# Kernel optimization log

Hardware: AMD Instinct MI355X
Metric: run time of the kernel (lower is better)

The kernel has to match this reference:

```python
import jax, jax.numpy as jnp
import numpy as np

N, E, H, NUM_RBF = 50000, 800000, 32, 32
D_IN = 2 * (NUM_RBF + H)  # 128: att_src(H) + att_dst(H) + rbf(2*NUM_RBF)
LN_EPS = 1e-5


def _decompose(t):
    # irreducible decomposition of [..., 3, 3] tensor
    eye = jnp.eye(3, dtype=t.dtype)
    I = jnp.mean(jnp.diagonal(t, axis1=-2, axis2=-1), axis=-1)[..., None, None] * eye
    A = 0.5 * (t - jnp.swapaxes(t, -1, -2))
    S = 0.5 * (t + jnp.swapaxes(t, -1, -2)) - I
    return I, A, S


def _tnorm(t):
    # squared Frobenius norm over last two dims -> [..., H]
    return (t ** 2).sum((-2, -1))


def _chan_lin(t, W):
    # nn.Linear over channel dim: t [N,H,3,3], W [H_out,H_in]
    return jnp.einsum('nhij,gh->ngij', t, W)


def setup_inputs() -> dict:
    key = jax.random.key(0)
    ks = jax.random.split(key, 12)

    def lin(k, o, i):
        return (jax.random.normal(k, (o, i), jnp.float32) / np.sqrt(i)).astype(jnp.float32)

    return {
        'X': jax.random.normal(ks[0], (N, H, 3, 3), jnp.float32),
        'rbf': jax.random.normal(ks[1], (E, 2 * NUM_RBF), jnp.float32),
        'dist': jax.random.uniform(ks[2], (E,), jnp.float32),
        'src': jax.random.randint(ks[3], (E,), 0, N),
        'dst': jax.random.randint(ks[4], (E,), 0, N),
        'Ws0': lin(ks[5], H, D_IN), 'b0': jnp.zeros((H,), jnp.float32),
        'Ws1': lin(ks[6], 2 * H, H), 'b1': jnp.zeros((2 * H,), jnp.float32),
        'Ws2': lin(ks[7], 3 * H, 2 * H), 'b2': jnp.zeros((3 * H,), jnp.float32),
        'Wt': (jax.random.normal(ks[8], (6, H, H), jnp.float32) / np.sqrt(H)).astype(jnp.float32),
        'ln_w': jnp.ones((3 * H,), jnp.float32), 'ln_b': jnp.zeros((3 * H,), jnp.float32),
        'lin_w': lin(ks[9], H, 3 * H), 'lin_b': jnp.zeros((H,), jnp.float32),
    }


def reference(X, rbf, dist, src, dst, Ws0, b0, Ws1, b1, Ws2, b2, Wt, ln_w, ln_b, lin_w, lin_b):
    n = X.shape[0]
    act = jax.nn.silu

    # atom_inf branch: per-node scalar attributes from tensor norms
    I, A, S = _decompose(X)
    x = jnp.concatenate([_tnorm(I), _tnorm(A), _tnorm(S)], axis=-1)  # [N, 3H]
    mu = x.mean(-1, keepdims=True)
    var = x.var(-1, keepdims=True)
    x = (x - mu) / jnp.sqrt(var + LN_EPS) * ln_w + ln_b
    att = act(x @ lin_w.T + lin_b)  # [N, H]

    # edge features: cat(att[src], att[dst], rbf) -> scalar MLP
    e = jnp.concatenate([att[src], att[dst], rbf], axis=-1)  # [E, D_IN]
    e = act(e @ Ws0.T + b0)
    e = act(e @ Ws1.T + b1)
    e = act(e @ Ws2.T + b2)  # [E, 3H]
    C = jnp.ones_like(dist)  # original code overwrites cutoff with ones
    e = (e * C[:, None]).reshape(e.shape[0], H, 3)  # [E, H, 3]

    # normalize node tensors, decompose, per-channel linear mix
    Xn = X / (_tnorm(X) + 1.0)[..., None, None]
    I, A, S = _decompose(Xn)
    I = _chan_lin(I, Wt[0])
    A = _chan_lin(A, Wt[1])
    S = _chan_lin(S, Wt[2])
    Y = I + A + S

    # tensor message passing: gather src, scale by edge factor, scatter-sum to dst
    def mp(T, f):
        return jax.ops.segment_sum(T[src] * f[:, :, None, None], dst, num_segments=n)

    msg = mp(I, e[..., 0]) + mp(A, e[..., 1]) + mp(S, e[..., 2])

    # O(3) group
    B1 = jnp.matmul(msg, Y)
    B2 = jnp.matmul(Y, msg)
    I, A, S = _decompose(B1 + B2)

    normp1 = (_tnorm(I + A + S) + 1.0)[..., None, None]
    I, A, S = I / normp1, A / normp1, S / normp1
    I = _chan_lin(I, Wt[3])
    A = _chan_lin(A, Wt[4])
    S = _chan_lin(S, Wt[5])
    dX = I + A + S
    X_out = Xn + dX + jnp.matmul(dX, dX)  # matrix_power(dX, 2)
    return X_out, e
```

## Files before the change

kernel.cpp:

```cpp
#include <hip/hip_runtime.h>
#include <math.h>

#define HC 32
#define NODE_PER_BLK 8

typedef _Float16 half8 __attribute__((ext_vector_type(8)));
typedef float float4v __attribute__((ext_vector_type(4)));

__device__ __forceinline__ float silu_f(float x) { return x / (1.0f + __expf(-x)); }

__device__ __forceinline__ unsigned int pk2(float a, float b) {
    union { _Float16 h[2]; unsigned int u; } t;
    t.h[0] = (_Float16)a; t.h[1] = (_Float16)b;
    return t.u;
}
__device__ __forceinline__ void unpk2(unsigned int u, float& a, float& b) {
    union { unsigned int u; _Float16 h[2]; } t;
    t.u = u;
    a = (float)t.h[0]; b = (float)t.h[1];
}

__device__ __forceinline__ void recon3(const float* c, float* T) {
    T[0] = c[0] + c[4];  T[1] = c[1] + c[5];  T[2] = c[2] + c[6];
    T[3] = -c[1] + c[5]; T[4] = c[0] + c[7];  T[5] = c[3] + c[8];
    T[6] = -c[2] + c[6]; T[7] = -c[3] + c[8]; T[8] = c[0] - c[4] - c[7];
}

__global__ void prep_weights(const float* __restrict__ Ws0, const float* __restrict__ Ws1,
                             const float* __restrict__ Ws2,
                             _Float16* __restrict__ wf1, _Float16* __restrict__ wf2,
                             _Float16* __restrict__ wf3) {
    int t = blockIdx.x * 256 + threadIdx.x;
    int j = t & 7;
    int lane = (t >> 3) & 63;
    int q = lane >> 4, r = lane & 15;
    if (t < 4096) {
        int fi = t >> 9, kt = fi >> 1, nt = fi & 1;
        wf1[t] = (_Float16)Ws0[(16 * nt + r) * 128 + 32 * kt + 8 * q + j];
    } else if (t < 6144) {
        int t2 = t - 4096;
        int nt = t2 >> 9;
        wf2[t2] = (_Float16)Ws1[(16 * nt + r) * 32 + 8 * q + j];
    } else if (t < 12288) {
        int t3 = t - 6144;
        int fi = t3 >> 9, kt = fi / 6, nt = fi % 6;
        wf3[t3] = (_Float16)Ws2[(16 * nt + r) * 64 + 32 * kt + 8 * q + j];
    }
}

__global__ void hist_kernel(const int* __restrict__ dst, int* __restrict__ cnt, int E) {
    int e = blockIdx.x * 256 + threadIdx.x;
    if (e < E) atomicAdd(&cnt[dst[e]], 1);
}

__global__ __launch_bounds__(1024) void scan_kernel(const int* __restrict__ cnt,
                                                    int* __restrict__ off,
                                                    int* __restrict__ cursor, int N) {
    __shared__ int s[1024];
    int carry = 0;
    for (int base = 0; base < N; base += 1024) {
        int i = base + threadIdx.x;
        int v = (i < N) ? cnt[i] : 0;
        s[threadIdx.x] = v;
        __syncthreads();
        #pragma unroll
        for (int o = 1; o < 1024; o <<= 1) {
            int t = (threadIdx.x >= o) ? s[threadIdx.x - o] : 0;
            __syncthreads();
            s[threadIdx.x] += t;
            __syncthreads();
        }
        int inc = s[threadIdx.x];
        int total = s[1023];
        if (i < N) {
            int ex = carry + inc - v;
            off[i] = ex;
            cursor[i] = ex;
        }
        __syncthreads();
        carry += total;
    }
    if (threadIdx.x == 0) off[N] = carry;
}

__global__ void scatter_kernel(const int* __restrict__ src, const int* __restrict__ dst,
                               int* __restrict__ cursor, int2* __restrict__ elist, int E) {
    int e = blockIdx.x * 256 + threadIdx.x;
    if (e >= E) return;
    int d = dst[e];
    int pos = atomicAdd(&cursor[d], 1);
    elist[pos] = make_int2(e, src[e]);
}

__global__ void node_prep(const float* __restrict__ X,
                          const float* __restrict__ lin_w, const float* __restrict__ lin_b,
                          const float* __restrict__ ln_w, const float* __restrict__ ln_b,
                          const float* __restrict__ Wt,
                          float* __restrict__ att, unsigned int* __restrict__ comp_g, int N) {
    __shared__ float sX[NODE_PER_BLK][96];
    __shared__ float sC[NODE_PER_BLK][HC * 9];
    int grp = threadIdx.x >> 5;
    int lane = threadIdx.x & 31;
    int n = blockIdx.x * NODE_PER_BLK + grp;
    bool valid = (n < N);

    float m = 0, a01 = 0, a02 = 0, a12 = 0, s00 = 0, s01 = 0, s02 = 0, s11 = 0, s12 = 0, s22 = 0;
    float tI = 0, tA = 0, tS = 0, tX = 0;
    if (valid) {
        const float* xp = X + (size_t)n * 288 + lane * 9;
        float t00 = xp[0], t01 = xp[1], t02 = xp[2];
        float t10 = xp[3], t11 = xp[4], t12 = xp[5];
        float t20 = xp[6], t21 = xp[7], t22 = xp[8];
        m = (t00 + t11 + t22) * (1.0f / 3.0f);
        a01 = 0.5f * (t01 - t10); a02 = 0.5f * (t02 - t20); a12 = 0.5f * (t12 - t21);
        s00 = t00 - m; s11 = t11 - m; s22 = t22 - m;
        s01 = 0.5f * (t01 + t10); s02 = 0.5f * (t02 + t20); s12 = 0.5f * (t12 + t21);
        tI = 3.0f * m * m;
        tA = 2.0f * (a01 * a01 + a02 * a02 + a12 * a12);
        tS = s00 * s00 + s11 * s11 + s22 * s22 + 2.0f * (s01 * s01 + s02 * s02 + s12 * s12);
        tX = tI + tA + tS;
    }
    float lsum = tI + tA + tS;
    #pragma unroll
    for (int o = 16; o; o >>= 1) lsum += __shfl_xor(lsum, o, 32);
    float mu = lsum * (1.0f / 96.0f);
    float d0 = tI - mu, d1 = tA - mu, d2 = tS - mu;
    float lsq = d0 * d0 + d1 * d1 + d2 * d2;
    #pragma unroll
    for (int o = 16; o; o >>= 1) lsq += __shfl_xor(lsq, o, 32);
    float rstd = rsqrtf(lsq * (1.0f / 96.0f) + 1e-5f);
    if (valid) {
        sX[grp][lane]      = d0 * rstd * ln_w[lane]      + ln_b[lane];
        sX[grp][32 + lane] = d1 * rstd * ln_w[32 + lane] + ln_b[32 + lane];
        sX[grp][64 + lane] = d2 * rstd * ln_w[64 + lane] + ln_b[64 + lane];
    }
    __syncthreads();
    if (valid) {
        float acc = lin_b[lane];
        const float* wr = lin_w + lane * 96;
        #pragma unroll
        for (int k = 0; k < 96; k++) acc += wr[k] * sX[grp][k];
        att[(size_t)n * 32 + lane] = silu_f(acc);
        float inv = 1.0f / (tX + 1.0f);
        float* cc = &sC[grp][lane * 9];
        cc[0] = m * inv;
        cc[1] = a01 * inv; cc[2] = a02 * inv; cc[3] = a12 * inv;
        cc[4] = s00 * inv; cc[5] = s01 * inv; cc[6] = s02 * inv;
        cc[7] = s11 * inv; cc[8] = s12 * inv;
    }
    __syncthreads();
    if (valid) {
        float o[9];
        #pragma unroll
        for (int c = 0; c < 9; c++) o[c] = 0.0f;
        const float* w0 = Wt + lane * 32;
        const float* w1 = Wt + 1024 + lane * 32;
        const float* w2 = Wt + 2048 + lane * 32;
        #pragma unroll
        for (int h = 0; h < 32; h++) {
            float wi = w0[h], wa = w1[h], ws = w2[h];
            const float* ch = &sC[grp][h * 9];
            o[0] += wi * ch[0];
            o[1] += wa * ch[1]; o[2] += wa * ch[2]; o[3] += wa * ch[3];
            o[4] += ws * ch[4]; o[5] += ws * ch[5]; o[6] += ws * ch[6];
            o[7] += ws * ch[7]; o[8] += ws * ch[8];
        }
        unsigned int* cgp = comp_g + (size_t)n * 160 + lane;
        cgp[0]   = pk2(o[0], o[1]);
        cgp[32]  = pk2(o[2], o[3]);
        cgp[64]  = pk2(o[4], o[5]);
        cgp[96]  = pk2(o[6], o[7]);
        cgp[128] = pk2(o[8], 0.0f);
    }
}

__device__ __forceinline__ half8 cvt8(const float* p) {
    half8 h;
    #pragma unroll
    for (int j = 0; j < 8; j++) h[j] = (_Float16)p[j];
    return h;
}

__global__ __launch_bounds__(256) void edge_mfma(
    const float* __restrict__ att, const float* __restrict__ rbf,
    const int* __restrict__ src, const int* __restrict__ dst,
    const _Float16* __restrict__ wf1, const _Float16* __restrict__ wf2,
    const _Float16* __restrict__ wf3,
    const float* __restrict__ b0, const float* __restrict__ b1, const float* __restrict__ b2,
    float* __restrict__ e_out, int E) {
    __shared__ _Float16 hbuf[4][16][72];
    int w = threadIdx.x >> 6;
    int lane = threadIdx.x & 63;
    int q = lane >> 4, r = lane & 15;
    int ebase = blockIdx.x * 64 + w * 16;
    int er = min(ebase + r, E - 1);
    int s = src[er], d = dst[er];

    half8 a0 = cvt8(att + (size_t)s * 32 + 8 * q);
    half8 a1 = cvt8(att + (size_t)d * 32 + 8 * q);
    half8 a2 = cvt8(rbf + (size_t)er * 64 + 8 * q);
    half8 a3 = cvt8(rbf + (size_t)er * 64 + 32 + 8 * q);

    const half8* W1 = (const half8*)wf1;
    float bn0 = b0[r], bn1 = b0[16 + r];
    float4v acc10 = {bn0, bn0, bn0, bn0};
    float4v acc11 = {bn1, bn1, bn1, bn1};
    acc10 = __builtin_amdgcn_mfma_f32_16x16x32_f16(a0, W1[0 * 64 + lane], acc10, 0, 0, 0);
    acc11 = __builtin_amdgcn_mfma_f32_16x16x32_f16(a0, W1[1 * 64 + lane], acc11, 0, 0, 0);
    acc10 = __builtin_amdgcn_mfma_f32_16x16x32_f16(a1, W1[2 * 64 + lane], acc10, 0, 0, 0);
    acc11 = __builtin_amdgcn_mfma_f32_16x16x32_f16(a1, W1[3 * 64 + lane], acc11, 0, 0, 0);
    acc10 = __builtin_amdgcn_mfma_f32_16x16x32_f16(a2, W1[4 * 64 + lane], acc10, 0, 0, 0);
    acc11 = __builtin_amdgcn_mfma_f32_16x16x32_f16(a2, W1[5 * 64 + lane], acc11, 0, 0, 0);
    acc10 = __builtin_amdgcn_mfma_f32_16x16x32_f16(a3, W1[6 * 64 + lane], acc10, 0, 0, 0);
    acc11 = __builtin_amdgcn_mfma_f32_16x16x32_f16(a3, W1[7 * 64 + lane], acc11, 0, 0, 0);
    #pragma unroll
    for (int reg = 0; reg < 4; reg++) {
        hbuf[w][4 * q + reg][r]      = (_Float16)silu_f(acc10[reg]);
        hbuf[w][4 * q + reg][16 + r] = (_Float16)silu_f(acc11[reg]);
    }

    half8 ah1 = *(const half8*)&hbuf[w][r][8 * q];
    const half8* W2 = (const half8*)wf2;
    float4v acc2[4];
    #pragma unroll
    for (int nt = 0; nt < 4; nt++) {
        float bb = b1[16 * nt + r];
        acc2[nt] = (float4v){bb, bb, bb, bb};
        acc2[nt] = __builtin_amdgcn_mfma_f32_16x16x32_f16(ah1, W2[nt * 64 + lane], acc2[nt], 0, 0, 0);
    }
    #pragma unroll
    for (int nt = 0; nt < 4; nt++) {
        #pragma unroll
        for (int reg = 0; reg < 4; reg++) {
            hbuf[w][4 * q + reg][16 * nt + r] = (_Float16)silu_f(acc2[nt][reg]);
        }
    }

    half8 ah20 = *(const half8*)&hbuf[w][r][8 * q];
    half8 ah21 = *(const half8*)&hbuf[w][r][32 + 8 * q];
    const half8* W3 = (const half8*)wf3;
    float4v acc3[6];
    #pragma unroll
    for (int nt = 0; nt < 6; nt++) {
        float bb = b2[16 * nt + r];
        acc3[nt] = (float4v){bb, bb, bb, bb};
        acc3[nt] = __builtin_amdgcn_mfma_f32_16x16x32_f16(ah20, W3[nt * 64 + lane], acc3[nt], 0, 0, 0);
        acc3[nt] = __builtin_amdgcn_mfma_f32_16x16x32_f16(ah21, W3[(6 + nt) * 64 + lane], acc3[nt], 0, 0, 0);
    }
    #pragma unroll
    for (int nt = 0; nt < 6; nt++) {
        #pragma unroll
        for (int reg = 0; reg < 4; reg++) {
            int ee = ebase + 4 * q + reg;
            if (ee < E) e_out[(size_t)ee * 96 + 16 * nt + r] = silu_f(acc3[nt][reg]);
        }
    }
}

__global__ void gather_final(const float* __restrict__ X,
                             const unsigned int* __restrict__ comp_g,
                             const float* __restrict__ e_out,
                             const int* __restrict__ off, const int2* __restrict__ elist,
                             const float* __restrict__ Wt,
                             float* __restrict__ Xout, int N) {
    __shared__ float sB[NODE_PER_BLK][HC * 9];
    int grp = threadIdx.x >> 5;
    int lane = threadIdx.x & 31;
    int n = blockIdx.x * NODE_PER_BLK + grp;
    bool valid = (n < N);

    float cm[9];
    #pragma unroll
    for (int c = 0; c < 9; c++) cm[c] = 0.0f;

    if (valid) {
        int start = off[n], end = off[n + 1];
        for (int idx = start; idx < end; idx++) {
            int2 es = elist[idx];
            const float* ep = e_out + (size_t)es.x * 96 + lane * 3;
            float e0 = ep[0], e1 = ep[1], e2 = ep[2];
            const unsigned int* cg = comp_g + (size_t)es.y * 160 + lane;
            float c0, c1, c2, c3, c4, c5, c6, c7, c8, cz;
            unpk2(cg[0], c0, c1);
            unpk2(cg[32], c2, c3);
            unpk2(cg[64], c4, c5);
            unpk2(cg[96], c6, c7);
            unpk2(cg[128], c8, cz);
            cm[0] += e0 * c0;
            cm[1] += e1 * c1; cm[2] += e1 * c2; cm[3] += e1 * c3;
            cm[4] += e2 * c4; cm[5] += e2 * c5; cm[6] += e2 * c6;
            cm[7] += e2 * c7; cm[8] += e2 * c8;
        }
    }

    if (valid) {
        float cy[9], cz;
        const unsigned int* cgn = comp_g + (size_t)n * 160 + lane;
        unpk2(cgn[0], cy[0], cy[1]);
        unpk2(cgn[32], cy[2], cy[3]);
        unpk2(cgn[64], cy[4], cy[5]);
        unpk2(cgn[96], cy[6], cy[7]);
        unpk2(cgn[128], cy[8], cz);
        float M[9], Y[9];
        recon3(cm, M);
        recon3(cy, Y);
        float B[9];
        #pragma unroll
        for (int i = 0; i < 3; i++) {
            #pragma unroll
            for (int j = 0; j < 3; j++) {
                float acc = 0.0f;
                #pragma unroll
                for (int k = 0; k < 3; k++)
                    acc += M[i * 3 + k] * Y[k * 3 + j] + Y[i * 3 + k] * M[k * 3 + j];
                B[i * 3 + j] = acc;
            }
        }
        float mB = (B[0] + B[4] + B[8]) * (1.0f / 3.0f);
        float tn = 1.0f;
        #pragma unroll
        for (int i = 0; i < 9; i++) tn += B[i] * B[i];
        float itn = 1.0f / tn;
        float* bb = &sB[grp][lane * 9];
        bb[0] = mB * itn;
        bb[1] = 0.5f * (B[1] - B[3]) * itn;
        bb[2] = 0.5f * (B[2] - B[6]) * itn;
        bb[3] = 0.5f * (B[5] - B[7]) * itn;
        bb[4] = (B[0] - mB) * itn;
        bb[5] = 0.5f * (B[1] + B[3]) * itn;
        bb[6] = 0.5f * (B[2] + B[6]) * itn;
        bb[7] = (B[4] - mB) * itn;
        bb[8] = 0.5f * (B[5] + B[7]) * itn;
    }
    __syncthreads();
    if (valid) {
        float o[9];
        #pragma unroll
        for (int c = 0; c < 9; c++) o[c] = 0.0f;
        const float* w3 = Wt + 3 * 1024 + lane * 32;
        const float* w4 = Wt + 4 * 1024 + lane * 32;
        const float* w5 = Wt + 5 * 1024 + lane * 32;
        #pragma unroll
        for (int h = 0; h < 32; h++) {
            float wi = w3[h], wa = w4[h], ws = w5[h];
            const float* ch = &sB[grp][h * 9];
            o[0] += wi * ch[0];
            o[1] += wa * ch[1]; o[2] += wa * ch[2]; o[3] += wa * ch[3];
            o[4] += ws * ch[4]; o[5] += ws * ch[5]; o[6] += ws * ch[6];
            o[7] += ws * ch[7]; o[8] += ws * ch[8];
        }
        float D[9];
        recon3(o, D);
        const float* xp = X + (size_t)n * 288 + lane * 9;
        float xv[9];
        float t = 0.0f;
        #pragma unroll
        for (int i = 0; i < 9; i++) { xv[i] = xp[i]; t += xv[i] * xv[i]; }
        float inv = 1.0f / (t + 1.0f);
        float P[9];
        #pragma unroll
        for (int i = 0; i < 3; i++) {
            #pragma unroll
            for (int j = 0; j < 3; j++) {
                float acc = 0.0f;
                #pragma unroll
                for (int k = 0; k < 3; k++) acc += D[i * 3 + k] * D[k * 3 + j];
                P[i * 3 + j] = acc;
            }
        }
        float* op = Xout + (size_t)n * 288 + lane * 9;
        #pragma unroll
        for (int i = 0; i < 9; i++) op[i] = xv[i] * inv + D[i] + P[i];
    }
}

extern "C" void kernel_launch(void* const* d_in, const int* in_sizes, int n_in,
                              void* d_out, int out_size, void* d_ws, size_t ws_size,
                              hipStream_t stream) {
    const float* X = (const float*)d_in[0];
    const float* rbf = (const float*)d_in[1];
    const int* src = (const int*)d_in[3];
    const int* dst = (const int*)d_in[4];
    const float* Ws0 = (const float*)d_in[5];
    const float* b0 = (const float*)d_in[6];
    const float* Ws1 = (const float*)d_in[7];
    const float* b1 = (const float*)d_in[8];
    const float* Ws2 = (const float*)d_in[9];
    const float* b2 = (const float*)d_in[10];
    const float* Wt = (const float*)d_in[11];
    const float* ln_w = (const float*)d_in[12];
    const float* ln_b = (const float*)d_in[13];
    const float* lin_w = (const float*)d_in[14];
    const float* lin_b = (const float*)d_in[15];

    int N = in_sizes[0] / 288;
    int E = in_sizes[1] / 64;

    float* Xout = (float*)d_out;
    float* e_out = (float*)d_out + (size_t)N * 288;

    float* att = (float*)d_ws;
    unsigned int* comp_g = (unsigned int*)(att + (size_t)N * 32);
    _Float16* wf1 = (_Float16*)(comp_g + (size_t)N * 160);
    _Float16* wf2 = wf1 + 4096;
    _Float16* wf3 = wf2 + 2048;
    int* cnt = (int*)(wf3 + 6144);
    int* off = cnt + N;
    int* cursor = off + N + 1;
    int2* elist = (int2*)(cursor + N + 1);

    hipMemsetAsync(cnt, 0, (size_t)N * sizeof(int), stream);
    prep_weights<<<48, 256, 0, stream>>>(Ws0, Ws1, Ws2, wf1, wf2, wf3);
    node_prep<<<(N + NODE_PER_BLK - 1) / NODE_PER_BLK, 256, 0, stream>>>(
        X, lin_w, lin_b, ln_w, ln_b, Wt, att, comp_g, N);
    hist_kernel<<<(E + 255) / 256, 256, 0, stream>>>(dst, cnt, E);
    scan_kernel<<<1, 1024, 0, stream>>>(cnt, off, cursor, N);
    scatter_kernel<<<(E + 255) / 256, 256, 0, stream>>>(src, dst, cursor, elist, E);
    edge_mfma<<<(E + 63) / 64, 256, 0, stream>>>(
        att, rbf, src, dst, wf1, wf2, wf3, b0, b1, b2, e_out, E);
    gather_final<<<(N + NODE_PER_BLK - 1) / NODE_PER_BLK, 256, 0, stream>>>(
        X, comp_g, e_out, off, elist, Wt, Xout, N);
}
```

Baseline: 704.2 us.

## Parallelize offset scan across blocks and split node edge gather across warps

Replaces the single-block serial prefix scan over node degrees with a three-pass multi-block scan (block sums, scan of sums, local scan plus offset). Reworks the gather kernel to assign one block per destination node, with eight warps striding over its incoming edges and reducing partial messages in shared memory. This targets the serial latency of the one-block scan and the per-node sequential edge loop. In exchange it adds two extra launches, launches one block per node, and leaves seven warps idle during the per-node epilogue.

```diff
diff --git a/kernel.cpp b/kernel.cpp
--- a/kernel.cpp
+++ b/kernel.cpp
@@ -53,34 +53,57 @@
     if (e < E) atomicAdd(&cnt[dst[e]], 1);
 }
 
-__global__ __launch_bounds__(1024) void scan_kernel(const int* __restrict__ cnt,
-                                                    int* __restrict__ off,
-                                                    int* __restrict__ cursor, int N) {
+__global__ __launch_bounds__(1024) void scan_a(const int* __restrict__ cnt,
+                                               int* __restrict__ bsum, int N) {
     __shared__ int s[1024];
-    int carry = 0;
-    for (int base = 0; base < N; base += 1024) {
-        int i = base + threadIdx.x;
-        int v = (i < N) ? cnt[i] : 0;
-        s[threadIdx.x] = v;
+    int i = blockIdx.x * 1024 + threadIdx.x;
+    s[threadIdx.x] = (i < N) ? cnt[i] : 0;
+    __syncthreads();
+    #pragma unroll
+    for (int o = 512; o; o >>= 1) {
+        if (threadIdx.x < o) s[threadIdx.x] += s[threadIdx.x + o];
         __syncthreads();
-        #pragma unroll
-        for (int o = 1; o < 1024; o <<= 1) {
-            int t = (threadIdx.x >= o) ? s[threadIdx.x - o] : 0;
-            __syncthreads();
-            s[threadIdx.x] += t;
-            __syncthreads();
-        }
-        int inc = s[threadIdx.x];
-        int total = s[1023];
-        if (i < N) {
-            int ex = carry + inc - v;
-            off[i] = ex;
-            cursor[i] = ex;
-        }
+    }
+    if (threadIdx.x == 0) bsum[blockIdx.x] = s[0];
+}
+
+__global__ __launch_bounds__(1024) void scan_b(int* __restrict__ bsum, int nb) {
+    __shared__ int s[1024];
+    int v = (threadIdx.x < nb) ? bsum[threadIdx.x] : 0;
+    s[threadIdx.x] = v;
+    __syncthreads();
+    #pragma unroll
+    for (int o = 1; o < 1024; o <<= 1) {
+        int t = (threadIdx.x >= o) ? s[threadIdx.x - o] : 0;
         __syncthreads();
-        carry += total;
-    }
-    if (threadIdx.x == 0) off[N] = carry;
+        s[threadIdx.x] += t;
+        __syncthreads();
+    }
+    if (threadIdx.x < nb) bsum[threadIdx.x] = s[threadIdx.x] - v;
+}
+
+__global__ __launch_bounds__(1024) void scan_c(const int* __restrict__ cnt,
+                                               const int* __restrict__ bsum,
+                                               int* __restrict__ off,
+                                               int* __restrict__ cursor, int N) {
+    __shared__ int s[1024];
+    int i = blockIdx.x * 1024 + threadIdx.x;
+    int v = (i < N) ? cnt[i] : 0;
+    s[threadIdx.x] = v;
+    __syncthreads();
+    #pragma unroll
+    for (int o = 1; o < 1024; o <<= 1) {
+        int t = (threadIdx.x >= o) ? s[threadIdx.x - o] : 0;
+        __syncthreads();
+        s[threadIdx.x] += t;
+        __syncthreads();
+    }
+    int ex = bsum[blockIdx.x] + s[threadIdx.x] - v;
+    if (i < N) {
+        off[i] = ex;
+        cursor[i] = ex;
+        if (i == N - 1) off[N] = ex + v;
+    }
 }
 
 __global__ void scatter_kernel(const int* __restrict__ src, const int* __restrict__ dst,
@@ -257,43 +280,53 @@
     }
 }
 
-__global__ void gather_final(const float* __restrict__ X,
-                             const unsigned int* __restrict__ comp_g,
-                             const float* __restrict__ e_out,
-                             const int* __restrict__ off, const int2* __restrict__ elist,
-                             const float* __restrict__ Wt,
-                             float* __restrict__ Xout, int N) {
-    __shared__ float sB[NODE_PER_BLK][HC * 9];
+__global__ __launch_bounds__(256) void gather_final(
+    const float* __restrict__ X, const unsigned int* __restrict__ comp_g,
+    const float* __restrict__ e_out,
+    const int* __restrict__ off, const int2* __restrict__ elist,
+    const float* __restrict__ Wt, float* __restrict__ Xout, int N) {
+    __shared__ float sM[8][288];
+    __shared__ float sB[288];
+    int n = blockIdx.x;
     int grp = threadIdx.x >> 5;
     int lane = threadIdx.x & 31;
-    int n = blockIdx.x * NODE_PER_BLK + grp;
-    bool valid = (n < N);
+    int start = off[n], end = off[n + 1];
 
     float cm[9];
     #pragma unroll
     for (int c = 0; c < 9; c++) cm[c] = 0.0f;
 
-    if (valid) {
-        int start = off[n], end = off[n + 1];
-        for (int idx = start; idx < end; idx++) {
-            int2 es = elist[idx];
-            const float* ep = e_out + (size_t)es.x * 96 + lane * 3;
-            float e0 = ep[0], e1 = ep[1], e2 = ep[2];
-            const unsigned int* cg = comp_g + (size_t)es.y * 160 + lane;
-            float c0, c1, c2, c3, c4, c5, c6, c7, c8, cz;
-            unpk2(cg[0], c0, c1);
-            unpk2(cg[32], c2, c3);
-            unpk2(cg[64], c4, c5);
-            unpk2(cg[96], c6, c7);
-            unpk2(cg[128], c8, cz);
-            cm[0] += e0 * c0;
-            cm[1] += e1 * c1; cm[2] += e1 * c2; cm[3] += e1 * c3;
-            cm[4] += e2 * c4; cm[5] += e2 * c5; cm[6] += e2 * c6;
-            cm[7] += e2 * c7; cm[8] += e2 * c8;
-        }
-    }
-
-    if (valid) {
+    for (int idx = start + grp; idx < end; idx += 8) {
+        int2 es = elist[idx];
+        const float* ep = e_out + (size_t)es.x * 96 + lane * 3;
+        float e0 = ep[0], e1 = ep[1], e2 = ep[2];
+        const unsigned int* cg = comp_g + (size_t)es.y * 160 + lane;
+        float c0, c1, c2, c3, c4, c5, c6, c7, c8, cz;
+        unpk2(cg[0], c0, c1);
+        unpk2(cg[32], c2, c3);
+        unpk2(cg[64], c4, c5);
+        unpk2(cg[96], c6, c7);
+        unpk2(cg[128], c8, cz);
+        cm[0] += e0 * c0;
+        cm[1] += e1 * c1; cm[2] += e1 * c2; cm[3] += e1 * c3;
+        cm[4] += e2 * c4; cm[5] += e2 * c5; cm[6] += e2 * c6;
+        cm[7] += e2 * c7; cm[8] += e2 * c8;
+    }
+    #pragma unroll
+    for (int c = 0; c < 9; c++) sM[grp][lane * 9 + c] = cm[c];
+    __syncthreads();
+    for (int t = threadIdx.x; t < 288; t += 256) {
+        float s = sM[0][t];
+        #pragma unroll
+        for (int g = 1; g < 8; g++) s += sM[g][t];
+        sM[0][t] = s;
+    }
+    __syncthreads();
+
+    if (grp == 0) {
+        float cmt[9];
+        #pragma unroll
+        for (int c = 0; c < 9; c++) cmt[c] = sM[0][lane * 9 + c];
         float cy[9], cz;
         const unsigned int* cgn = comp_g + (size_t)n * 160 + lane;
         unpk2(cgn[0], cy[0], cy[1]);
@@ -302,7 +335,7 @@
         unpk2(cgn[96], cy[6], cy[7]);
         unpk2(cgn[128], cy[8], cz);
         float M[9], Y[9];
-        recon3(cm, M);
+        recon3(cmt, M);
         recon3(cy, Y);
         float B[9];
         #pragma unroll
@@ -321,7 +354,7 @@
         #pragma unroll
         for (int i = 0; i < 9; i++) tn += B[i] * B[i];
         float itn = 1.0f / tn;
-        float* bb = &sB[grp][lane * 9];
+        float* bb = &sB[lane * 9];
         bb[0] = mB * itn;
         bb[1] = 0.5f * (B[1] - B[3]) * itn;
         bb[2] = 0.5f * (B[2] - B[6]) * itn;
@@ -333,7 +366,7 @@
         bb[8] = 0.5f * (B[5] + B[7]) * itn;
     }
     __syncthreads();
-    if (valid) {
+    if (grp == 0) {
         float o[9];
         #pragma unroll
         for (int c = 0; c < 9; c++) o[c] = 0.0f;
@@ -343,7 +376,7 @@
         #pragma unroll
         for (int h = 0; h < 32; h++) {
             float wi = w3[h], wa = w4[h], ws = w5[h];
-            const float* ch = &sB[grp][h * 9];
+            const float* ch = &sB[h * 9];
             o[0] += wi * ch[0];
             o[1] += wa * ch[1]; o[2] += wa * ch[2]; o[3] += wa * ch[3];
             o[4] += ws * ch[4]; o[5] += ws * ch[5]; o[6] += ws * ch[6];
@@ -353,10 +386,10 @@
         recon3(o, D);
         const float* xp = X + (size_t)n * 288 + lane * 9;
         float xv[9];
-        float t = 0.0f;
-        #pragma unroll
-        for (int i = 0; i < 9; i++) { xv[i] = xp[i]; t += xv[i] * xv[i]; }
-        float inv = 1.0f / (t + 1.0f);
+        float tt = 0.0f;
+        #pragma unroll
+        for (int i = 0; i < 9; i++) { xv[i] = xp[i]; tt += xv[i] * xv[i]; }
+        float inv = 1.0f / (tt + 1.0f);
         float P[9];
         #pragma unroll
         for (int i = 0; i < 3; i++) {
@@ -407,17 +440,22 @@
     int* cnt = (int*)(wf3 + 6144);
     int* off = cnt + N;
     int* cursor = off + N + 1;
-    int2* elist = (int2*)(cursor + N + 1);
+    int* bsum = cursor + N + 1;
+    int2* elist = (int2*)(bsum + 1026);
+
+    int nb = (N + 1023) / 1024;
 
     hipMemsetAsync(cnt, 0, (size_t)N * sizeof(int), stream);
     prep_weights<<<48, 256, 0, stream>>>(Ws0, Ws1, Ws2, wf1, wf2, wf3);
     node_prep<<<(N + NODE_PER_BLK - 1) / NODE_PER_BLK, 256, 0, stream>>>(
         X, lin_w, lin_b, ln_w, ln_b, Wt, att, comp_g, N);
     hist_kernel<<<(E + 255) / 256, 256, 0, stream>>>(dst, cnt, E);
-    scan_kernel<<<1, 1024, 0, stream>>>(cnt, off, cursor, N);
+    scan_a<<<nb, 1024, 0, stream>>>(cnt, bsum, N);
+    scan_b<<<1, 1024, 0, stream>>>(bsum, nb);
+    scan_c<<<nb, 1024, 0, stream>>>(cnt, bsum, off, cursor, N);
     scatter_kernel<<<(E + 255) / 256, 256, 0, stream>>>(src, dst, cursor, elist, E);
     edge_mfma<<<(E + 63) / 64, 256, 0, stream>>>(
         att, rbf, src, dst, wf1, wf2, wf3, b0, b1, b2, e_out, E);
-    gather_final<<<(N + NODE_PER_BLK - 1) / NODE_PER_BLK, 256, 0, stream>>>(
+    gather_final<<<N, 256, 0, stream>>>(
         X, comp_g, e_out, off, elist, Wt, Xout, N);
 }
```

Result: faster. 665.9 us (-5.4%).
